# Kernel tuning notes

Measured on AMD Instinct MI355X. Metric: run time of the kernel, lower is better.

The kernel has to match this reference:

```python
import jax, jax.numpy as jnp
import numpy as np

N_NODES = 50000
N_EDGES = 1600000
N_GRAPHS = 128
IN_C, HID, N_CLS = 128, 256, 10


def setup_inputs() -> dict:
    key = jax.random.key(0)
    ks = jax.random.split(key, 8)
    x = jax.random.normal(ks[0], (N_NODES, IN_C), dtype=jnp.float32)
    edge_index = jax.random.randint(ks[1], (2, N_EDGES), 0, N_NODES, dtype=jnp.int64)
    batch = jnp.sort(jax.random.randint(ks[2], (N_NODES,), 0, N_GRAPHS, dtype=jnp.int64))
    def glorot(k, shape):
        lim = np.sqrt(6.0 / (shape[0] + shape[1]))
        return jax.random.uniform(k, shape, jnp.float32, -lim, lim)
    return {
        "x": x, "edge_index": edge_index, "batch": batch,
        "W1": glorot(ks[3], (IN_C, HID)), "b1": jnp.zeros((HID,), jnp.float32),
        "W2": glorot(ks[4], (HID, HID)), "b2": jnp.zeros((HID,), jnp.float32),
        "Wl1": glorot(ks[5], (HID, 64)), "bl1": jnp.zeros((64,), jnp.float32),
        "Wl2": glorot(ks[6], (64, N_CLS)), "bl2": jnp.zeros((N_CLS,), jnp.float32),
    }


def _gcn_conv(x, row, col, deg_inv_sqrt, W, b):
    h = x @ W                                  # [N, out]
    norm = deg_inv_sqrt[row] * deg_inv_sqrt[col]   # [E]
    msg = h[row] * norm[:, None]                   # gather + scale
    agg = jax.ops.segment_sum(msg, col, num_segments=x.shape[0])
    agg = agg + h * (deg_inv_sqrt * deg_inv_sqrt)[:, None]  # self-loop term (norm = 1/deg)
    return agg + b


def reference(x, edge_index, batch, W1, b1, W2, b2, Wl1, bl1, Wl2, bl2):
    N = x.shape[0]
    row, col = edge_index[0], edge_index[1]
    # degree including self-loop, computed on target nodes (PyG convention)
    deg = jax.ops.segment_sum(jnp.ones((row.shape[0],), x.dtype), col, num_segments=N) + 1.0
    deg_inv_sqrt = jax.lax.rsqrt(deg)

    h = jax.nn.relu(_gcn_conv(x, row, col, deg_inv_sqrt, W1, b1))
    h = jax.nn.relu(_gcn_conv(h, row, col, deg_inv_sqrt, W2, b2))

    # global_mean_pool over batch ids
    sums = jax.ops.segment_sum(h, batch, num_segments=N_GRAPHS)
    cnts = jax.ops.segment_sum(jnp.ones((N,), h.dtype), batch, num_segments=N_GRAPHS)
    g = sums / jnp.maximum(cnts, 1.0)[:, None]     # [G, HID]

    g = jax.nn.relu(g @ Wl1 + bl1)
    return jax.nn.log_softmax(g @ Wl2 + bl2, axis=1)
```

## Files before the change

kernel.cpp:

```cpp
#include <hip/hip_runtime.h>
#include <hip/hip_bf16.h>
#include <math.h>

#define NN 50000
#define NG 128
#define INC 128
#define HIDC 256
#define NCLS 10

#define NBLK 256
#define BSH 8
#define NB 196

typedef _Float16 h8_t __attribute__((ext_vector_type(8)));
typedef __attribute__((ext_vector_type(4))) float f4_t;

__device__ inline f4_t mfma16(h8_t a, h8_t b, f4_t c) {
  return __builtin_amdgcn_mfma_f32_16x16x32_f16(a, b, c, 0, 0, 0);
}

__device__ inline ushort f2h(float f) {
  _Float16 h = (_Float16)f; return *(ushort*)&h;
}
__device__ inline float h2f(ushort u) {
  _Float16 h = *(_Float16*)&u; return (float)h;
}
__device__ inline float h_lo(unsigned u) {
  union { unsigned v; _Float16 h[2]; } c; c.v = u; return (float)c.h[0];
}
__device__ inline float h_hi(unsigned u) {
  union { unsigned v; _Float16 h[2]; } c; c.v = u; return (float)c.h[1];
}
__device__ inline unsigned packh(float a, float b) {
  return (unsigned)f2h(a) | ((unsigned)f2h(b) << 16);
}

__device__ inline void gload_lds16(const void* g, void* l) {
  __builtin_amdgcn_global_load_lds(
      (const __attribute__((address_space(1))) unsigned int*)g,
      (__attribute__((address_space(3))) unsigned int*)l, 16, 0, 0);
}

__global__ __launch_bounds__(256) void edge_hist(const int* __restrict__ ecol,
                                                 int* __restrict__ hist, int E, int chunk) {
  __shared__ int h[NB];
  int blk = blockIdx.x;
  for (int i = threadIdx.x; i < NB; i += 256) h[i] = 0;
  __syncthreads();
  int e0 = blk * chunk, e1 = min(e0 + chunk, E);
  for (int e = e0 + threadIdx.x; e < e1; e += 256)
    atomicAdd(&h[ecol[e] >> BSH], 1);
  __syncthreads();
  for (int i = threadIdx.x; i < NB; i += 256) hist[i * NBLK + blk] = h[i];
}

__global__ __launch_bounds__(256) void edge_partition(const int* __restrict__ erow,
                                                      const int* __restrict__ ecol,
                                                      const int* __restrict__ histBase,
                                                      unsigned* __restrict__ part,
                                                      int E, int chunk) {
  __shared__ int cur[NB];
  int blk = blockIdx.x;
  for (int i = threadIdx.x; i < NB; i += 256) cur[i] = histBase[i * NBLK + blk];
  __syncthreads();
  int e0 = blk * chunk, e1 = min(e0 + chunk, E);
  for (int e = e0 + threadIdx.x; e < e1; e += 256) {
    int c = ecol[e];
    int b = c >> BSH;
    int pos = atomicAdd(&cur[b], 1);
    part[pos] = ((unsigned)erow[e] << 8) | (unsigned)(c & 255);
  }
}

__global__ __launch_bounds__(256) void bucket_deg_dis(const unsigned* __restrict__ part,
                                                      const int* __restrict__ histBase,
                                                      int* __restrict__ deg,
                                                      float* __restrict__ dis, int N) {
  __shared__ int cnt[256];
  int b = blockIdx.x;
  cnt[threadIdx.x] = 0;
  __syncthreads();
  int s0 = histBase[b * NBLK];
  int s1 = histBase[(b + 1) * NBLK];
  for (int e = s0 + threadIdx.x; e < s1; e += 256)
    atomicAdd(&cnt[part[e] & 255], 1);
  __syncthreads();
  int node = (b << BSH) + threadIdx.x;
  if (node < N) {
    int d = cnt[threadIdx.x];
    deg[node] = d;
    dis[node] = rsqrtf((float)d + 1.0f);
  }
}

__global__ __launch_bounds__(256) void bucket_csr_ew(const unsigned* __restrict__ part,
                                                     const int* __restrict__ histBase,
                                                     const int* __restrict__ offsets,
                                                     const float* __restrict__ dis,
                                                     unsigned* __restrict__ ew, int N) {
  __shared__ int cur[256];
  __shared__ float sdis[256];
  int b = blockIdx.x;
  int node = (b << BSH) + threadIdx.x;
  cur[threadIdx.x] = (node < N) ? offsets[node] : 0;
  sdis[threadIdx.x] = (node < N) ? dis[node] : 0.0f;
  __syncthreads();
  int s0 = histBase[b * NBLK];
  int s1 = histBase[(b + 1) * NBLK];
  for (int e = s0 + threadIdx.x; e < s1; e += 256) {
    unsigned pv = part[e];
    int c = pv & 255;
    int r = (int)(pv >> 8);
    int pos = atomicAdd(&cur[c], 1);
    float w = dis[r] * sdis[c];
    ew[pos] = ((unsigned)r << 16) | (unsigned)f2h(w);
  }
}

#define SCAN_T 256
#define SCAN_V 8
#define SCAN_VPB (SCAN_T * SCAN_V)

__global__ __launch_bounds__(SCAN_T) void scanA(const int* __restrict__ deg,
                                                int* __restrict__ offsets,
                                                int* __restrict__ blockTotals, int n) {
  __shared__ int sm[SCAN_T];
  int b = blockIdx.x;
  int t = threadIdx.x;
  int base = b * SCAN_VPB + t * SCAN_V;
  int v[SCAN_V];
  int run = 0;
  #pragma unroll
  for (int j = 0; j < SCAN_V; ++j) {
    int idx = base + j;
    int d = (idx < n) ? deg[idx] : 0;
    run += d;
    v[j] = run;
  }
  sm[t] = run;
  __syncthreads();
  #pragma unroll
  for (int off = 1; off < SCAN_T; off <<= 1) {
    int x = (t >= off) ? sm[t - off] : 0;
    __syncthreads();
    sm[t] += x;
    __syncthreads();
  }
  int excl = (t == 0) ? 0 : sm[t - 1];
  #pragma unroll
  for (int j = 0; j < SCAN_V; ++j) {
    int idx = base + j;
    if (idx < n) offsets[idx + 1] = v[j] + excl;
  }
  if (t == SCAN_T - 1) blockTotals[b] = sm[t];
}

__global__ void scanB(int* __restrict__ blockTotals, int nb) {
  if (threadIdx.x == 0 && blockIdx.x == 0) {
    int run = 0;
    for (int i = 0; i < nb; ++i) {
      int v = blockTotals[i];
      blockTotals[i] = run;
      run += v;
    }
  }
}

__global__ void scanC(int* __restrict__ offsets, const int* __restrict__ blockTotals, int n) {
  int stride = gridDim.x * blockDim.x;
  for (int i = blockIdx.x * blockDim.x + threadIdx.x; i < n; i += stride) {
    offsets[i + 1] += blockTotals[i / SCAN_VPB];
    if (i == 0) offsets[0] = 0;
  }
}

__global__ void cast_x_cb(const float* __restrict__ x, unsigned* __restrict__ xcb, int N) {
  int t = blockIdx.x * 256 + threadIdx.x;
  if (t >= N * 64) return;
  int n = t >> 6, pp = t & 63;
  float v0 = x[(long)n * 128 + 2 * pp];
  float v1 = x[(long)n * 128 + 2 * pp + 1];
  xcb[((long)(pp >> 4) * N + n) * 16 + (pp & 15)] = packh(v0, v1);
}

__global__ void transpose_cast2(const float* __restrict__ W1, ushort* __restrict__ W1T,
                                const float* __restrict__ W2, ushort* __restrict__ W2T) {
  int idx = blockIdx.x * blockDim.x + threadIdx.x;
  if (idx < INC * HIDC) {
    int k = idx / HIDC, n = idx % HIDC;
    W1T[(long)n * INC + k] = f2h(W1[idx]);
  }
  int i2 = idx - INC * HIDC;
  if (i2 >= 0 && i2 < HIDC * HIDC) {
    int k = i2 / HIDC, n = i2 % HIDC;
    W2T[(long)n * HIDC + k] = f2h(W2[i2]);
  }
}

template <int MODE>
__global__ __launch_bounds__(256) void aggregate_cb(
    const uint2* __restrict__ xcb, const float* __restrict__ dis,
    const int* __restrict__ offsets, const unsigned* __restrict__ ew,
    uint2* __restrict__ outcb, int N) {
  int blk = blockIdx.x;
  int slice, nb;
  if (MODE == 0) { slice = blk & 7; nb = blk >> 3; }
  else           { slice = (blk >> 1) & 3; nb = ((blk >> 3) << 1) | (blk & 1); }
  int node = nb * 32 + (threadIdx.x >> 3);
  if (node >= N) return;
  int cl = threadIdx.x & 7;
  const uint2* xs = xcb + (long)slice * N * 8;
  uint2* os = outcb + (long)slice * N * 8;
  float di = dis[node];
  float dd = di * di;
  uint2 sv = xs[node * 8 + cl];
  float a0 = h_lo(sv.x) * dd;
  float a1 = h_hi(sv.x) * dd;
  float a2 = h_lo(sv.y) * dd;
  float a3 = h_hi(sv.y) * dd;
  float b0 = 0, b1 = 0, b2 = 0, b3 = 0;
  float c0 = 0, c1 = 0, c2 = 0, c3 = 0;
  float d0 = 0, d1 = 0, d2 = 0, d3 = 0;
  int e = offsets[node], eE = offsets[node + 1];
  for (; e + 7 < eE; e += 8) {
    unsigned p0 = ew[e],     p1 = ew[e + 1], p2 = ew[e + 2], p3 = ew[e + 3];
    unsigned p4 = ew[e + 4], p5 = ew[e + 5], p6 = ew[e + 6], p7 = ew[e + 7];
    uint2 v0 = xs[(p0 >> 16) * 8 + cl];
    uint2 v1 = xs[(p1 >> 16) * 8 + cl];
    uint2 v2 = xs[(p2 >> 16) * 8 + cl];
    uint2 v3 = xs[(p3 >> 16) * 8 + cl];
    uint2 v4 = xs[(p4 >> 16) * 8 + cl];
    uint2 v5 = xs[(p5 >> 16) * 8 + cl];
    uint2 v6 = xs[(p6 >> 16) * 8 + cl];
    uint2 v7 = xs[(p7 >> 16) * 8 + cl];
    float w0 = h2f((ushort)p0), w1 = h2f((ushort)p1);
    float w2 = h2f((ushort)p2), w3 = h2f((ushort)p3);
    float w4 = h2f((ushort)p4), w5 = h2f((ushort)p5);
    float w6 = h2f((ushort)p6), w7 = h2f((ushort)p7);
    a0 = fmaf(h_lo(v0.x), w0, a0); a1 = fmaf(h_hi(v0.x), w0, a1);
    a2 = fmaf(h_lo(v0.y), w0, a2); a3 = fmaf(h_hi(v0.y), w0, a3);
    b0 = fmaf(h_lo(v1.x), w1, b0); b1 = fmaf(h_hi(v1.x), w1, b1);
    b2 = fmaf(h_lo(v1.y), w1, b2); b3 = fmaf(h_hi(v1.y), w1, b3);
    c0 = fmaf(h_lo(v2.x), w2, c0); c1 = fmaf(h_hi(v2.x), w2, c1);
    c2 = fmaf(h_lo(v2.y), w2, c2); c3 = fmaf(h_hi(v2.y), w2, c3);
    d0 = fmaf(h_lo(v3.x), w3, d0); d1 = fmaf(h_hi(v3.x), w3, d1);
    d2 = fmaf(h_lo(v3.y), w3, d2); d3 = fmaf(h_hi(v3.y), w3, d3);
    a0 = fmaf(h_lo(v4.x), w4, a0); a1 = fmaf(h_hi(v4.x), w4, a1);
    a2 = fmaf(h_lo(v4.y), w4, a2); a3 = fmaf(h_hi(v4.y), w4, a3);
    b0 = fmaf(h_lo(v5.x), w5, b0); b1 = fmaf(h_hi(v5.x), w5, b1);
    b2 = fmaf(h_lo(v5.y), w5, b2); b3 = fmaf(h_hi(v5.y), w5, b3);
    c0 = fmaf(h_lo(v6.x), w6, c0); c1 = fmaf(h_hi(v6.x), w6, c1);
    c2 = fmaf(h_lo(v6.y), w6, c2); c3 = fmaf(h_hi(v6.y), w6, c3);
    d0 = fmaf(h_lo(v7.x), w7, d0); d1 = fmaf(h_hi(v7.x), w7, d1);
    d2 = fmaf(h_lo(v7.y), w7, d2); d3 = fmaf(h_hi(v7.y), w7, d3);
  }
  for (; e < eE; ++e) {
    unsigned p0 = ew[e];
    uint2 v0 = xs[(p0 >> 16) * 8 + cl];
    float w0 = h2f((ushort)p0);
    a0 = fmaf(h_lo(v0.x), w0, a0); a1 = fmaf(h_hi(v0.x), w0, a1);
    a2 = fmaf(h_lo(v0.y), w0, a2); a3 = fmaf(h_hi(v0.y), w0, a3);
  }
  a0 += b0 + c0 + d0; a1 += b1 + c1 + d1;
  a2 += b2 + c2 + d2; a3 += b3 + c3 + d3;
  os[node * 8 + cl] = make_uint2(packh(a0, a1), packh(a2, a3));
}

template <int K, bool OUTCB>
__global__ __launch_bounds__(256) void gemm_mfma(
    const ushort* __restrict__ A, const ushort* __restrict__ WT,
    const float* __restrict__ bias, ushort* __restrict__ outb, int M) {
  __shared__ ushort smem[16384];
  const int tid = threadIdx.x;
  const int lane = tid & 63;
  const int wave = tid >> 6;
  const int wm = wave >> 1, wn = wave & 1;
  const int m0 = blockIdx.x * 128;
  const int n0 = blockIdx.y * 128;

  f4_t acc[4][4] = {};

  for (int k0 = 0; k0 < K; k0 += 64) {
    __syncthreads();
    #pragma unroll
    for (int is = 0; is < 4; ++is) {
      int s = is * 256 + tid;
      int row = s >> 3;
      int ch = (s & 7) ^ (row & 7);
      int k = k0 + ch * 8;
      long grow = m0 + row; if (grow > M - 1) grow = M - 1;
      const ushort* g = A + ((long)(k >> 5) * M + grow) * 32 + (k & 31);
      gload_lds16(g, &smem[(is * 256 + wave * 64) * 8]);
    }
    #pragma unroll
    for (int is = 0; is < 4; ++is) {
      int s = is * 256 + tid;
      int row = s >> 3;
      int ch = (s & 7) ^ (row & 7);
      const ushort* g = WT + (long)(n0 + row) * K + k0 + ch * 8;
      gload_lds16(g, &smem[8192 + (is * 256 + wave * 64) * 8]);
    }
    asm volatile("s_waitcnt vmcnt(0)" ::: "memory");
    __syncthreads();
    #pragma unroll
    for (int ks = 0; ks < 2; ++ks) {
      h8_t af[4], bfr[4];
      #pragma unroll
      for (int mi = 0; mi < 4; ++mi) {
        int row = wm * 64 + mi * 16 + (lane & 15);
        int ch = (ks * 4 + (lane >> 4)) ^ (row & 7);
        af[mi] = *(const h8_t*)(&smem[row * 64 + ch * 8]);
      }
      #pragma unroll
      for (int ni = 0; ni < 4; ++ni) {
        int row = wn * 64 + ni * 16 + (lane & 15);
        int ch = (ks * 4 + (lane >> 4)) ^ (row & 7);
        bfr[ni] = *(const h8_t*)(&smem[8192 + row * 64 + ch * 8]);
      }
      #pragma unroll
      for (int mi = 0; mi < 4; ++mi)
        #pragma unroll
        for (int ni = 0; ni < 4; ++ni)
          acc[mi][ni] = mfma16(af[mi], bfr[ni], acc[mi][ni]);
    }
  }
  #pragma unroll
  for (int ni = 0; ni < 4; ++ni) {
    int col = n0 + wn * 64 + ni * 16 + (lane & 15);
    float bb = bias[col];
    #pragma unroll
    for (int mi = 0; mi < 4; ++mi) {
      #pragma unroll
      for (int r = 0; r < 4; ++r) {
        int row = m0 + wm * 64 + mi * 16 + (lane >> 4) * 4 + r;
        if (row < M) {
          float v = fmaxf(acc[mi][ni][r] + bb, 0.0f);
          if (OUTCB)
            outb[((long)(col >> 5) * M + row) * 32 + (col & 31)] = f2h(v);
          else
            outb[(long)row * HIDC + col] = f2h(v);
        }
      }
    }
  }
}

__global__ void find_bounds(const int* __restrict__ batch, int* __restrict__ gstart, int n) {
  int stride = gridDim.x * blockDim.x;
  for (int i = blockIdx.x * blockDim.x + threadIdx.x; i < n; i += stride) {
    int b = batch[i];
    if (i == 0) {
      for (int g = 0; g <= b; ++g) gstart[g] = 0;
    } else {
      int pb = batch[i - 1];
      if (pb != b)
        for (int g = pb + 1; g <= b; ++g) gstart[g] = i;
    }
    if (i == n - 1) {
      for (int g = b + 1; g <= NG; ++g) gstart[g] = n;
    }
  }
}

#define POOL_SPLIT 8
__global__ __launch_bounds__(HIDC) void pool_range_f16(const ushort* __restrict__ h,
                                                       const int* __restrict__ gstart,
                                                       float* __restrict__ gsum) {
  int g = blockIdx.x;
  int s = blockIdx.y;
  int c = threadIdx.x;
  int s0 = gstart[g], s1 = gstart[g + 1];
  int len = s1 - s0;
  int chunk = (len + POOL_SPLIT - 1) / POOL_SPLIT;
  int i0 = s0 + s * chunk;
  int i1 = min(i0 + chunk, s1);
  float acc = 0.0f;
  for (int i = i0; i < i1; ++i) acc += h2f(h[(long)i * HIDC + c]);
  if (i1 > i0) atomicAdd(&gsum[g * HIDC + c], acc);
}

__global__ __launch_bounds__(64) void mlp_kernel(
    const float* __restrict__ gsum, const int* __restrict__ gstart,
    const float* __restrict__ Wl1, const float* __restrict__ bl1,
    const float* __restrict__ Wl2, const float* __restrict__ bl2,
    float* __restrict__ out) {
  __shared__ float g[HIDC];
  __shared__ float hid[64];
  __shared__ float logits[NCLS];
  __shared__ float red[2];
  int i = blockIdx.x;
  int t = threadIdx.x;
  int cnt = gstart[i + 1] - gstart[i];
  float inv = 1.0f / fmaxf((float)cnt, 1.0f);
  for (int c = t; c < HIDC; c += 64) g[c] = gsum[i * HIDC + c] * inv;
  __syncthreads();
  float acc = bl1[t];
  for (int c = 0; c < HIDC; ++c) acc = fmaf(g[c], Wl1[c * 64 + t], acc);
  hid[t] = fmaxf(acc, 0.0f);
  __syncthreads();
  if (t < NCLS) {
    float l = bl2[t];
    for (int c = 0; c < 64; ++c) l = fmaf(hid[c], Wl2[c * NCLS + t], l);
    logits[t] = l;
  }
  __syncthreads();
  if (t == 0) {
    float m = -1e30f;
    for (int k = 0; k < NCLS; ++k) m = fmaxf(m, logits[k]);
    float s = 0.f;
    for (int k = 0; k < NCLS; ++k) s += expf(logits[k] - m);
    red[0] = m;
    red[1] = logf(s);
  }
  __syncthreads();
  if (t < NCLS) out[i * NCLS + t] = logits[t] - red[0] - red[1];
}

extern "C" void kernel_launch(void* const* d_in, const int* in_sizes, int n_in,
                              void* d_out, int out_size, void* d_ws, size_t ws_size,
                              hipStream_t stream) {
  const float* x = (const float*)d_in[0];
  const int* edge_index = (const int*)d_in[1];
  const int* batch = (const int*)d_in[2];
  const float* W1 = (const float*)d_in[3];
  const float* b1 = (const float*)d_in[4];
  const float* W2 = (const float*)d_in[5];
  const float* b2 = (const float*)d_in[6];
  const float* Wl1 = (const float*)d_in[7];
  const float* bl1 = (const float*)d_in[8];
  const float* Wl2 = (const float*)d_in[9];
  const float* bl2 = (const float*)d_in[10];
  float* out = (float*)d_out;

  const int N = in_sizes[0] / INC;
  const int E = in_sizes[1] / 2;
  const int* erow = edge_index;
  const int* ecol = edge_index + E;

  char* p = (char*)d_ws;
  auto alloc = [&](size_t bytes) {
    void* r = (void*)p;
    p += (bytes + 255) & ~(size_t)255;
    return r;
  };
  int* deg = (int*)alloc((size_t)N * 4);
  float* dis = (float*)alloc((size_t)N * 4);
  int* offsets = (int*)alloc((size_t)(N + 1) * 4);
  unsigned* ew = (unsigned*)alloc((size_t)E * 4);
  unsigned* part = (unsigned*)alloc((size_t)E * 4);
  int* hist = (int*)alloc((size_t)(NB * NBLK) * 4);
  int* histBase = (int*)alloc((size_t)(NB * NBLK + 1) * 4);
  float* gsum = (float*)alloc((size_t)NG * HIDC * 4);
  int* gstart = (int*)alloc((size_t)(NG + 1) * 4);
  int* blockTotals = (int*)alloc((size_t)256 * 4);
  ushort* W1T = (ushort*)alloc((size_t)INC * HIDC * 2);
  ushort* W2T = (ushort*)alloc((size_t)HIDC * HIDC * 2);
  unsigned* x_cb = (unsigned*)alloc((size_t)N * INC * 2);
  unsigned* agg1_cb = (unsigned*)alloc((size_t)N * INC * 2);
  unsigned* h1_cb = (unsigned*)alloc((size_t)N * HIDC * 2);
  unsigned* agg2_cb = (unsigned*)alloc((size_t)N * HIDC * 2);
  ushort* h2 = (ushort*)x_cb;

  hipMemsetAsync(gsum, 0, (size_t)NG * HIDC * 4, stream);

  const int chunk = (E + NBLK - 1) / NBLK;
  edge_hist<<<NBLK, 256, 0, stream>>>(ecol, hist, E, chunk);
  {
    const int nh = NB * NBLK;
    const int nbh = (nh + SCAN_VPB - 1) / SCAN_VPB;
    scanA<<<nbh, SCAN_T, 0, stream>>>(hist, histBase, blockTotals, nh);
    scanB<<<1, 64, 0, stream>>>(blockTotals, nbh);
    scanC<<<(nh + 255) / 256, 256, 0, stream>>>(histBase, blockTotals, nh);
  }
  edge_partition<<<NBLK, 256, 0, stream>>>(erow, ecol, histBase, part, E, chunk);
  bucket_deg_dis<<<NB, 256, 0, stream>>>(part, histBase, deg, dis, N);
  {
    const int nb = (N + SCAN_VPB - 1) / SCAN_VPB;
    scanA<<<nb, SCAN_T, 0, stream>>>(deg, offsets, blockTotals, N);
    scanB<<<1, 64, 0, stream>>>(blockTotals, nb);
    scanC<<<(N + 255) / 256, 256, 0, stream>>>(offsets, blockTotals, N);
  }
  bucket_csr_ew<<<NB, 256, 0, stream>>>(part, histBase, offsets, dis, ew, N);

  cast_x_cb<<<(N * 64 + 255) / 256, 256, 0, stream>>>(x, x_cb, N);
  {
    int tot = INC * HIDC + HIDC * HIDC;
    transpose_cast2<<<(tot + 255) / 256, 256, 0, stream>>>(W1, W1T, W2, W2T);
  }

  {
    const int nb2 = (N + 63) / 64;
    aggregate_cb<1><<<nb2 << 3, 256, 0, stream>>>(
        (const uint2*)x_cb, dis, offsets, ew, (uint2*)agg1_cb, N);
  }
  {
    dim3 grid((N + 127) / 128, HIDC / 128);
    gemm_mfma<INC, true><<<grid, 256, 0, stream>>>(
        (const ushort*)agg1_cb, W1T, b1, (ushort*)h1_cb, N);
  }
  {
    const int nodeblks = (N + 31) / 32;
    aggregate_cb<0><<<nodeblks << 3, 256, 0, stream>>>(
        (const uint2*)h1_cb, dis, offsets, ew, (uint2*)agg2_cb, N);
  }
  {
    dim3 grid((N + 127) / 128, HIDC / 128);
    gemm_mfma<HIDC, false><<<grid, 256, 0, stream>>>(
        (const ushort*)agg2_cb, W2T, b2, h2, N);
  }
  find_bounds<<<(N + 255) / 256, 256, 0, stream>>>(batch, gstart, N);
  {
    dim3 pgrid(NG, POOL_SPLIT);
    pool_range_f16<<<pgrid, HIDC, 0, stream>>>(h2, gstart, gsum);
  }
  mlp_kernel<<<NG, 64, 0, stream>>>(gsum, gstart, Wl1, bl1, Wl2, bl2, out);
}
```

Before: 401.2 us.

## Cut kernel launches and switch aggregation to packed fp16 math

Node offsets are now computed by an in-block scan inside the bucket degree kernel, which removes the separate three-kernel global scan over degrees. The x and weight cast kernels are merged into one launch. find_bounds is replaced by binary searches on the sorted batch array inside the pool and MLP kernels. The aggregation kernel now accumulates in packed fp16 (h2 vector FMA) instead of fp32, which halves the ALU work but lowers accumulation precision on high-degree nodes.

```diff
diff --git a/kernel.cpp b/kernel.cpp
--- a/kernel.cpp
+++ b/kernel.cpp
@@ -13,6 +13,7 @@
 #define NB 196
 
 typedef _Float16 h8_t __attribute__((ext_vector_type(8)));
+typedef _Float16 h2_t __attribute__((ext_vector_type(2)));
 typedef __attribute__((ext_vector_type(4))) float f4_t;
 
 __device__ inline f4_t mfma16(h8_t a, h8_t b, f4_t c) {
@@ -25,20 +26,20 @@
 __device__ inline float h2f(ushort u) {
   _Float16 h = *(_Float16*)&u; return (float)h;
 }
-__device__ inline float h_lo(unsigned u) {
-  union { unsigned v; _Float16 h[2]; } c; c.v = u; return (float)c.h[0];
-}
-__device__ inline float h_hi(unsigned u) {
-  union { unsigned v; _Float16 h[2]; } c; c.v = u; return (float)c.h[1];
-}
-__device__ inline unsigned packh(float a, float b) {
-  return (unsigned)f2h(a) | ((unsigned)f2h(b) << 16);
-}
+
+union U2 { uint2 u; struct { h2_t x, y; } h; };
+union UW { unsigned u; h2_t h; };
 
 __device__ inline void gload_lds16(const void* g, void* l) {
   __builtin_amdgcn_global_load_lds(
       (const __attribute__((address_space(1))) unsigned int*)g,
       (__attribute__((address_space(3))) unsigned int*)l, 16, 0, 0);
+}
+
+__device__ inline int lbound(const int* __restrict__ a, int n, int key) {
+  int lo = 0, hi = n;
+  while (lo < hi) { int m = (lo + hi) >> 1; if (a[m] < key) lo = m + 1; else hi = m; }
+  return lo;
 }
 
 __global__ __launch_bounds__(256) void edge_hist(const int* __restrict__ ecol,
@@ -72,24 +73,37 @@
   }
 }
 
-__global__ __launch_bounds__(256) void bucket_deg_dis(const unsigned* __restrict__ part,
+__global__ __launch_bounds__(256) void bucket_off_dis(const unsigned* __restrict__ part,
                                                       const int* __restrict__ histBase,
-                                                      int* __restrict__ deg,
+                                                      int* __restrict__ offsets,
                                                       float* __restrict__ dis, int N) {
   __shared__ int cnt[256];
-  int b = blockIdx.x;
-  cnt[threadIdx.x] = 0;
+  __shared__ int sm[256];
+  int b = blockIdx.x, t = threadIdx.x;
+  cnt[t] = 0;
   __syncthreads();
   int s0 = histBase[b * NBLK];
   int s1 = histBase[(b + 1) * NBLK];
-  for (int e = s0 + threadIdx.x; e < s1; e += 256)
+  for (int e = s0 + t; e < s1; e += 256)
     atomicAdd(&cnt[part[e] & 255], 1);
   __syncthreads();
-  int node = (b << BSH) + threadIdx.x;
+  int v = cnt[t];
+  sm[t] = v;
+  __syncthreads();
+  #pragma unroll
+  for (int off = 1; off < 256; off <<= 1) {
+    int x = (t >= off) ? sm[t - off] : 0;
+    __syncthreads();
+    sm[t] += x;
+    __syncthreads();
+  }
+  int excl = (t == 0) ? 0 : sm[t - 1];
+  int node = (b << BSH) + t;
   if (node < N) {
-    int d = cnt[threadIdx.x];
-    deg[node] = d;
-    dis[node] = rsqrtf((float)d + 1.0f);
+    offsets[node] = s0 + excl;
+    dis[node] = rsqrtf((float)v + 1.0f);
+  } else if (node == N) {
+    offsets[N] = s0 + excl;
   }
 }
 
@@ -174,24 +188,27 @@
   }
 }
 
-__global__ void cast_x_cb(const float* __restrict__ x, unsigned* __restrict__ xcb, int N) {
-  int t = blockIdx.x * 256 + threadIdx.x;
-  if (t >= N * 64) return;
-  int n = t >> 6, pp = t & 63;
-  float v0 = x[(long)n * 128 + 2 * pp];
-  float v1 = x[(long)n * 128 + 2 * pp + 1];
-  xcb[((long)(pp >> 4) * N + n) * 16 + (pp & 15)] = packh(v0, v1);
-}
-
-__global__ void transpose_cast2(const float* __restrict__ W1, ushort* __restrict__ W1T,
-                                const float* __restrict__ W2, ushort* __restrict__ W2T) {
-  int idx = blockIdx.x * blockDim.x + threadIdx.x;
-  if (idx < INC * HIDC) {
-    int k = idx / HIDC, n = idx % HIDC;
-    W1T[(long)n * INC + k] = f2h(W1[idx]);
-  }
-  int i2 = idx - INC * HIDC;
-  if (i2 >= 0 && i2 < HIDC * HIDC) {
+__global__ void cast_all(const float* __restrict__ x, unsigned* __restrict__ xcb,
+                         const float* __restrict__ W1, ushort* __restrict__ W1T,
+                         const float* __restrict__ W2, ushort* __restrict__ W2T, int N) {
+  int idx = blockIdx.x * 256 + threadIdx.x;
+  int nx = N * 64;
+  if (idx < nx) {
+    int n = idx >> 6, pp = idx & 63;
+    float v0 = x[(long)n * 128 + 2 * pp];
+    float v1 = x[(long)n * 128 + 2 * pp + 1];
+    xcb[((long)(pp >> 4) * N + n) * 16 + (pp & 15)] =
+        (unsigned)f2h(v0) | ((unsigned)f2h(v1) << 16);
+    return;
+  }
+  int i1 = idx - nx;
+  if (i1 < INC * HIDC) {
+    int k = i1 / HIDC, n = i1 % HIDC;
+    W1T[(long)n * INC + k] = f2h(W1[i1]);
+    return;
+  }
+  int i2 = i1 - INC * HIDC;
+  if (i2 < HIDC * HIDC) {
     int k = i2 / HIDC, n = i2 % HIDC;
     W2T[(long)n * HIDC + k] = f2h(W2[i2]);
   }
@@ -212,58 +229,53 @@
   const uint2* xs = xcb + (long)slice * N * 8;
   uint2* os = outcb + (long)slice * N * 8;
   float di = dis[node];
-  float dd = di * di;
-  uint2 sv = xs[node * 8 + cl];
-  float a0 = h_lo(sv.x) * dd;
-  float a1 = h_hi(sv.x) * dd;
-  float a2 = h_lo(sv.y) * dd;
-  float a3 = h_hi(sv.y) * dd;
-  float b0 = 0, b1 = 0, b2 = 0, b3 = 0;
-  float c0 = 0, c1 = 0, c2 = 0, c3 = 0;
-  float d0 = 0, d1 = 0, d2 = 0, d3 = 0;
+  _Float16 ddh = (_Float16)(di * di);
+  h2_t dd2 = {ddh, ddh};
+  U2 sv; sv.u = xs[node * 8 + cl];
+  h2_t ax = sv.h.x * dd2, ay = sv.h.y * dd2;
+  h2_t bx = {0, 0}, by = {0, 0};
+  h2_t cx = {0, 0}, cy = {0, 0};
+  h2_t dx = {0, 0}, dy = {0, 0};
   int e = offsets[node], eE = offsets[node + 1];
   for (; e + 7 < eE; e += 8) {
     unsigned p0 = ew[e],     p1 = ew[e + 1], p2 = ew[e + 2], p3 = ew[e + 3];
     unsigned p4 = ew[e + 4], p5 = ew[e + 5], p6 = ew[e + 6], p7 = ew[e + 7];
-    uint2 v0 = xs[(p0 >> 16) * 8 + cl];
-    uint2 v1 = xs[(p1 >> 16) * 8 + cl];
-    uint2 v2 = xs[(p2 >> 16) * 8 + cl];
-    uint2 v3 = xs[(p3 >> 16) * 8 + cl];
-    uint2 v4 = xs[(p4 >> 16) * 8 + cl];
-    uint2 v5 = xs[(p5 >> 16) * 8 + cl];
-    uint2 v6 = xs[(p6 >> 16) * 8 + cl];
-    uint2 v7 = xs[(p7 >> 16) * 8 + cl];
-    float w0 = h2f((ushort)p0), w1 = h2f((ushort)p1);
-    float w2 = h2f((ushort)p2), w3 = h2f((ushort)p3);
-    float w4 = h2f((ushort)p4), w5 = h2f((ushort)p5);
-    float w6 = h2f((ushort)p6), w7 = h2f((ushort)p7);
-    a0 = fmaf(h_lo(v0.x), w0, a0); a1 = fmaf(h_hi(v0.x), w0, a1);
-    a2 = fmaf(h_lo(v0.y), w0, a2); a3 = fmaf(h_hi(v0.y), w0, a3);
-    b0 = fmaf(h_lo(v1.x), w1, b0); b1 = fmaf(h_hi(v1.x), w1, b1);
-    b2 = fmaf(h_lo(v1.y), w1, b2); b3 = fmaf(h_hi(v1.y), w1, b3);
-    c0 = fmaf(h_lo(v2.x), w2, c0); c1 = fmaf(h_hi(v2.x), w2, c1);
-    c2 = fmaf(h_lo(v2.y), w2, c2); c3 = fmaf(h_hi(v2.y), w2, c3);
-    d0 = fmaf(h_lo(v3.x), w3, d0); d1 = fmaf(h_hi(v3.x), w3, d1);
-    d2 = fmaf(h_lo(v3.y), w3, d2); d3 = fmaf(h_hi(v3.y), w3, d3);
-    a0 = fmaf(h_lo(v4.x), w4, a0); a1 = fmaf(h_hi(v4.x), w4, a1);
-    a2 = fmaf(h_lo(v4.y), w4, a2); a3 = fmaf(h_hi(v4.y), w4, a3);
-    b0 = fmaf(h_lo(v5.x), w5, b0); b1 = fmaf(h_hi(v5.x), w5, b1);
-    b2 = fmaf(h_lo(v5.y), w5, b2); b3 = fmaf(h_hi(v5.y), w5, b3);
-    c0 = fmaf(h_lo(v6.x), w6, c0); c1 = fmaf(h_hi(v6.x), w6, c1);
-    c2 = fmaf(h_lo(v6.y), w6, c2); c3 = fmaf(h_hi(v6.y), w6, c3);
-    d0 = fmaf(h_lo(v7.x), w7, d0); d1 = fmaf(h_hi(v7.x), w7, d1);
-    d2 = fmaf(h_lo(v7.y), w7, d2); d3 = fmaf(h_hi(v7.y), w7, d3);
+    U2 v0, v1, v2, v3, v4, v5, v6, v7;
+    v0.u = xs[(p0 >> 16) * 8 + cl];
+    v1.u = xs[(p1 >> 16) * 8 + cl];
+    v2.u = xs[(p2 >> 16) * 8 + cl];
+    v3.u = xs[(p3 >> 16) * 8 + cl];
+    v4.u = xs[(p4 >> 16) * 8 + cl];
+    v5.u = xs[(p5 >> 16) * 8 + cl];
+    v6.u = xs[(p6 >> 16) * 8 + cl];
+    v7.u = xs[(p7 >> 16) * 8 + cl];
+    UW q0, q1, q2, q3, q4, q5, q6, q7;
+    q0.u = p0; q1.u = p1; q2.u = p2; q3.u = p3;
+    q4.u = p4; q5.u = p5; q6.u = p6; q7.u = p7;
+    h2_t w0 = {q0.h[0], q0.h[0]}, w1 = {q1.h[0], q1.h[0]};
+    h2_t w2 = {q2.h[0], q2.h[0]}, w3 = {q3.h[0], q3.h[0]};
+    h2_t w4 = {q4.h[0], q4.h[0]}, w5 = {q5.h[0], q5.h[0]};
+    h2_t w6 = {q6.h[0], q6.h[0]}, w7 = {q7.h[0], q7.h[0]};
+    ax = v0.h.x * w0 + ax; ay = v0.h.y * w0 + ay;
+    bx = v1.h.x * w1 + bx; by = v1.h.y * w1 + by;
+    cx = v2.h.x * w2 + cx; cy = v2.h.y * w2 + cy;
+    dx = v3.h.x * w3 + dx; dy = v3.h.y * w3 + dy;
+    ax = v4.h.x * w4 + ax; ay = v4.h.y * w4 + ay;
+    bx = v5.h.x * w5 + bx; by = v5.h.y * w5 + by;
+    cx = v6.h.x * w6 + cx; cy = v6.h.y * w6 + cy;
+    dx = v7.h.x * w7 + dx; dy = v7.h.y * w7 + dy;
   }
   for (; e < eE; ++e) {
     unsigned p0 = ew[e];
-    uint2 v0 = xs[(p0 >> 16) * 8 + cl];
-    float w0 = h2f((ushort)p0);
-    a0 = fmaf(h_lo(v0.x), w0, a0); a1 = fmaf(h_hi(v0.x), w0, a1);
-    a2 = fmaf(h_lo(v0.y), w0, a2); a3 = fmaf(h_hi(v0.y), w0, a3);
-  }
-  a0 += b0 + c0 + d0; a1 += b1 + c1 + d1;
-  a2 += b2 + c2 + d2; a3 += b3 + c3 + d3;
-  os[node * 8 + cl] = make_uint2(packh(a0, a1), packh(a2, a3));
+    U2 v0; v0.u = xs[(p0 >> 16) * 8 + cl];
+    UW q0; q0.u = p0;
+    h2_t w0 = {q0.h[0], q0.h[0]};
+    ax = v0.h.x * w0 + ax; ay = v0.h.y * w0 + ay;
+  }
+  ax = ax + bx + cx + dx;
+  ay = ay + by + cy + dy;
+  U2 o; o.h.x = ax; o.h.y = ay;
+  os[node * 8 + cl] = o.u;
 }
 
 template <int K, bool OUTCB>
@@ -345,31 +357,15 @@
   }
 }
 
-__global__ void find_bounds(const int* __restrict__ batch, int* __restrict__ gstart, int n) {
-  int stride = gridDim.x * blockDim.x;
-  for (int i = blockIdx.x * blockDim.x + threadIdx.x; i < n; i += stride) {
-    int b = batch[i];
-    if (i == 0) {
-      for (int g = 0; g <= b; ++g) gstart[g] = 0;
-    } else {
-      int pb = batch[i - 1];
-      if (pb != b)
-        for (int g = pb + 1; g <= b; ++g) gstart[g] = i;
-    }
-    if (i == n - 1) {
-      for (int g = b + 1; g <= NG; ++g) gstart[g] = n;
-    }
-  }
-}
-
 #define POOL_SPLIT 8
 __global__ __launch_bounds__(HIDC) void pool_range_f16(const ushort* __restrict__ h,
-                                                       const int* __restrict__ gstart,
-                                                       float* __restrict__ gsum) {
+                                                       const int* __restrict__ batch,
+                                                       float* __restrict__ gsum, int N) {
   int g = blockIdx.x;
   int s = blockIdx.y;
   int c = threadIdx.x;
-  int s0 = gstart[g], s1 = gstart[g + 1];
+  int s0 = lbound(batch, N, g);
+  int s1 = lbound(batch, N, g + 1);
   int len = s1 - s0;
   int chunk = (len + POOL_SPLIT - 1) / POOL_SPLIT;
   int i0 = s0 + s * chunk;
@@ -380,17 +376,17 @@
 }
 
 __global__ __launch_bounds__(64) void mlp_kernel(
-    const float* __restrict__ gsum, const int* __restrict__ gstart,
+    const float* __restrict__ gsum, const int* __restrict__ batch,
     const float* __restrict__ Wl1, const float* __restrict__ bl1,
     const float* __restrict__ Wl2, const float* __restrict__ bl2,
-    float* __restrict__ out) {
+    float* __restrict__ out, int N) {
   __shared__ float g[HIDC];
   __shared__ float hid[64];
   __shared__ float logits[NCLS];
   __shared__ float red[2];
   int i = blockIdx.x;
   int t = threadIdx.x;
-  int cnt = gstart[i + 1] - gstart[i];
+  int cnt = lbound(batch, N, i + 1) - lbound(batch, N, i);
   float inv = 1.0f / fmaxf((float)cnt, 1.0f);
   for (int c = t; c < HIDC; c += 64) g[c] = gsum[i * HIDC + c] * inv;
   __syncthreads();
@@ -443,7 +439,6 @@
     p += (bytes + 255) & ~(size_t)255;
     return r;
   };
-  int* deg = (int*)alloc((size_t)N * 4);
   float* dis = (float*)alloc((size_t)N * 4);
   int* offsets = (int*)alloc((size_t)(N + 1) * 4);
   unsigned* ew = (unsigned*)alloc((size_t)E * 4);
@@ -451,7 +446,6 @@
   int* hist = (int*)alloc((size_t)(NB * NBLK) * 4);
   int* histBase = (int*)alloc((size_t)(NB * NBLK + 1) * 4);
   float* gsum = (float*)alloc((size_t)NG * HIDC * 4);
-  int* gstart = (int*)alloc((size_t)(NG + 1) * 4);
   int* blockTotals = (int*)alloc((size_t)256 * 4);
   ushort* W1T = (ushort*)alloc((size_t)INC * HIDC * 2);
   ushort* W2T = (ushort*)alloc((size_t)HIDC * HIDC * 2);
@@ -473,19 +467,12 @@
     scanC<<<(nh + 255) / 256, 256, 0, stream>>>(histBase, blockTotals, nh);
   }
   edge_partition<<<NBLK, 256, 0, stream>>>(erow, ecol, histBase, part, E, chunk);
-  bucket_deg_dis<<<NB, 256, 0, stream>>>(part, histBase, deg, dis, N);
-  {
-    const int nb = (N + SCAN_VPB - 1) / SCAN_VPB;
-    scanA<<<nb, SCAN_T, 0, stream>>>(deg, offsets, blockTotals, N);
-    scanB<<<1, 64, 0, stream>>>(blockTotals, nb);
-    scanC<<<(N + 255) / 256, 256, 0, stream>>>(offsets, blockTotals, N);
-  }
+  bucket_off_dis<<<NB, 256, 0, stream>>>(part, histBase, offsets, dis, N);
   bucket_csr_ew<<<NB, 256, 0, stream>>>(part, histBase, offsets, dis, ew, N);
 
-  cast_x_cb<<<(N * 64 + 255) / 256, 256, 0, stream>>>(x, x_cb, N);
-  {
-    int tot = INC * HIDC + HIDC * HIDC;
-    transpose_cast2<<<(tot + 255) / 256, 256, 0, stream>>>(W1, W1T, W2, W2T);
+  {
+    int tot = N * 64 + INC * HIDC + HIDC * HIDC;
+    cast_all<<<(tot + 255) / 256, 256, 0, stream>>>(x, x_cb, W1, W1T, W2, W2T, N);
   }
 
   {
@@ -508,10 +495,9 @@
     gemm_mfma<HIDC, false><<<grid, 256, 0, stream>>>(
         (const ushort*)agg2_cb, W2T, b2, h2, N);
   }
-  find_bounds<<<(N + 255) / 256, 256, 0, stream>>>(batch, gstart, N);
   {
     dim3 pgrid(NG, POOL_SPLIT);
-    pool_range_f16<<<pgrid, HIDC, 0, stream>>>(h2, gstart, gsum);
-  }
-  mlp_kernel<<<NG, 64, 0, stream>>>(gsum, gstart, Wl1, bl1, Wl2, bl2, out);
-}
+    pool_range_f16<<<pgrid, HIDC, 0, stream>>>(h2, batch, gsum, N);
+  }
+  mlp_kernel<<<NG, 64, 0, stream>>>(gsum, batch, Wl1, bl1, Wl2, bl2, out, N);
+}
```

New measurement: 396.8 us. Within noise of the previous version (-1.1%).
